# Performance work log

Measured on AMD Instinct MI355X. Metric: run time of the kernel, lower is better.

Reference implementation:

```python
import jax, jax.numpy as jnp
import numpy as np

N_NODES = 50000
N_EDGES = 600000
D_IN = 128
D_OUT = 128


def setup_inputs() -> dict:
    key = jax.random.key(0)
    ks = jax.random.split(key, 6)
    gain = float(np.sqrt(2.0))  # relu gain for xavier init
    lim = gain * np.sqrt(6.0 / (D_IN + D_IN))
    pool_w = jax.random.uniform(ks[0], (D_IN, D_IN), jnp.float32, -lim, lim)
    lim2 = gain * np.sqrt(6.0 / (D_IN + D_OUT))
    lin_w = jax.random.uniform(ks[1], (D_OUT, D_IN), jnp.float32, -lim2, lim2)
    return {
        "node_feats": jax.random.normal(ks[2], (N_NODES, D_IN), jnp.float32),
        "src": jax.random.randint(ks[3], (N_EDGES,), 0, N_NODES, jnp.int32),
        "dst": jax.random.randint(ks[4], (N_EDGES,), 0, N_NODES, jnp.int32),
        "e_weight": jax.random.uniform(ks[5], (N_EDGES,), jnp.float32),
        "pool_w": pool_w,
        "pool_b": jnp.zeros((D_IN,), jnp.float32),
        "lin_w": lin_w,
        "lin_b": jnp.zeros((D_OUT,), jnp.float32),
        "bias": jnp.zeros((D_OUT,), jnp.float32),
    }


def reference(node_feats, src, dst, e_weight, pool_w, pool_b, lin_w, lin_b, bias):
    # maxpool aggregator: h_src = relu(pool(x) + pool_bias)   [N, D_IN]
    h_src = jax.nn.relu(node_feats @ pool_w.T + pool_b)
    # u_mul_e message: gather src features, scale by edge weight  [E, D_IN]
    m = h_src[src] * e_weight[:, None]
    # fn.max reduce per destination node; empty mailboxes -> 0
    h_new = jax.ops.segment_max(m, dst, num_segments=N_NODES)
    h_new = jnp.where(jnp.isfinite(h_new), h_new, 0.0)
    # final linear (+its bias) + extra bias parameter
    return h_new @ lin_w.T + lin_b + bias
```

## Files before the change

### kernel.cpp

```cpp
#include <hip/hip_runtime.h>
#include <hip/hip_bf16.h>

#define NN 50000
#define NE 600000
#define DD 128
#define CAP 48

typedef __attribute__((ext_vector_type(8))) short short8_t;
typedef __attribute__((ext_vector_type(4))) short short4_t;
typedef __attribute__((ext_vector_type(4))) float f32x4;

__device__ __forceinline__ short f2bf(float f) {
    union { float f; unsigned u; } v; v.f = f;
    unsigned r = (v.u + 0x7FFFu + ((v.u >> 16) & 1u)) >> 16;
    return (short)r;
}
__device__ __forceinline__ float bflo(unsigned x) { return __uint_as_float(x << 16); }
__device__ __forceinline__ float bfhi(unsigned x) { return __uint_as_float(x & 0xffff0000u); }

template<bool RELU, bool B2, bool IN_BF, bool OUT_BF>
__global__ __launch_bounds__(512) void gemm128(const void* __restrict__ Av,
        const float* __restrict__ W, const float* __restrict__ b1,
        const float* __restrict__ b2, void* __restrict__ outv, int M)
{
    __shared__ short aL[128 * 128];
    __shared__ short wL[128 * 128];
    const int tid = threadIdx.x;
    const int m0 = blockIdx.x * 128;

    if (IN_BF) {
        const unsigned short* A = (const unsigned short*)Av;
        #pragma unroll
        for (int i = 0; i < 4; ++i) {
            int flat = i * 4096 + tid * 8;
            int row = flat >> 7, k = flat & 127;
            int gr = m0 + row;
            short8_t s8 = {0,0,0,0,0,0,0,0};
            if (gr < M) s8 = *(const short8_t*)(A + (size_t)gr * 128 + k);
            *(short8_t*)(aL + ((row * 128 + k) ^ ((row & 7) << 3))) = s8;
        }
    } else {
        const float* A = (const float*)Av;
        #pragma unroll
        for (int i = 0; i < 8; ++i) {
            int flat = i * 2048 + tid * 4;
            int row = flat >> 7, k = flat & 127;
            int gr = m0 + row;
            float4 v = make_float4(0.f, 0.f, 0.f, 0.f);
            if (gr < M) v = *(const float4*)(A + (size_t)gr * 128 + k);
            short4_t s4 = { f2bf(v.x), f2bf(v.y), f2bf(v.z), f2bf(v.w) };
            *(short4_t*)(aL + ((row * 128 + k) ^ ((row & 7) << 3))) = s4;
        }
    }
    #pragma unroll
    for (int i = 0; i < 8; ++i) {
        int flat = i * 2048 + tid * 4;
        int row = flat >> 7, k = flat & 127;
        float4 v = *(const float4*)(W + flat);
        short4_t s4 = { f2bf(v.x), f2bf(v.y), f2bf(v.z), f2bf(v.w) };
        *(short4_t*)(wL + ((row * 128 + k) ^ ((row & 7) << 3))) = s4;
    }
    __syncthreads();

    const int lane = tid & 63, wid = tid >> 6;
    const int l15 = lane & 15, lhi = lane >> 4;
    const int r0 = wid * 16;
    f32x4 acc[8];
    #pragma unroll
    for (int t = 0; t < 8; ++t) acc[t] = f32x4{0.f, 0.f, 0.f, 0.f};

    #pragma unroll
    for (int kk = 0; kk < 4; ++kk) {
        const int k0 = kk * 32 + lhi * 8;
        const int ar = r0 + l15;
        short8_t a = *(short8_t*)(aL + ((ar * 128 + k0) ^ ((ar & 7) << 3)));
        #pragma unroll
        for (int t = 0; t < 8; ++t) {
            const int br = t * 16 + l15;
            short8_t b = *(short8_t*)(wL + ((br * 128 + k0) ^ ((br & 7) << 3)));
            acc[t] = __builtin_amdgcn_mfma_f32_16x16x32_bf16(a, b, acc[t], 0, 0, 0);
        }
    }

    #pragma unroll
    for (int t = 0; t < 8; ++t) {
        const int c = t * 16 + l15;
        float add = b1[c];
        if (B2) add += b2[c];
        #pragma unroll
        for (int i = 0; i < 4; ++i) {
            int r = m0 + r0 + lhi * 4 + i;
            if (r < M) {
                float v = acc[t][i] + add;
                if (RELU) v = fmaxf(v, 0.f);
                if (OUT_BF) ((unsigned short*)outv)[(size_t)r * 128 + c] = (unsigned short)f2bf(v);
                else        ((float*)outv)[(size_t)r * 128 + c] = v;
            }
        }
    }
}

__global__ __launch_bounds__(256) void bucket(const int* __restrict__ src,
        const int* __restrict__ dst, const float* __restrict__ ew,
        int* __restrict__ counts, int2* __restrict__ edges)
{
    int e = blockIdx.x * 256 + threadIdx.x;
    if (e >= NE) return;
    int d = dst[e];
    int pos = atomicAdd(&counts[d], 1);
    if (pos < CAP) edges[(size_t)d * CAP + pos] = make_int2(src[e], __float_as_int(ew[e]));
}

__global__ __launch_bounds__(256) void node_max(const unsigned short* __restrict__ hb,
        const int* __restrict__ counts, const int2* __restrict__ edges,
        unsigned short* __restrict__ hnew)
{
    int node = blockIdx.x * 4 + (threadIdx.x >> 6);
    if (node >= NN) return;
    int lane = threadIdx.x & 63;
    int deg = min(counts[node], CAP);
    const int2* ep = edges + (size_t)node * CAP;
    int2 e = make_int2(0, 0);
    if (lane < deg) e = ep[lane];
    float a0 = 0.f, a1 = 0.f, b0 = 0.f, b1v = 0.f;
    for (int j = 0; j < deg; j += 16) {
        #pragma unroll
        for (int u = 0; u < 16; u += 2) {
            int i0 = j + u, i1 = j + u + 1;
            int s0 = __shfl(e.x, i0 & 63);
            int s1 = __shfl(e.x, i1 & 63);
            float w0 = __int_as_float(__shfl(e.y, i0 & 63));
            float w1 = __int_as_float(__shfl(e.y, i1 & 63));
            w0 = (i0 < deg) ? w0 : 0.f;
            w1 = (i1 < deg) ? w1 : 0.f;
            unsigned x0 = *(const unsigned*)(hb + (size_t)s0 * 128 + lane * 2);
            unsigned x1 = *(const unsigned*)(hb + (size_t)s1 * 128 + lane * 2);
            a0 = fmaxf(a0, bflo(x0) * w0); a1 = fmaxf(a1, bfhi(x0) * w0);
            b0 = fmaxf(b0, bflo(x1) * w1); b1v = fmaxf(b1v, bfhi(x1) * w1);
        }
    }
    float m0 = fmaxf(a0, b0), m1 = fmaxf(a1, b1v);
    unsigned o = ((unsigned)(unsigned short)f2bf(m1) << 16) | (unsigned short)f2bf(m0);
    *(unsigned*)(hnew + (size_t)node * 128 + lane * 2) = o;
}

extern "C" void kernel_launch(void* const* d_in, const int* in_sizes, int n_in,
                              void* d_out, int out_size, void* d_ws, size_t ws_size,
                              hipStream_t stream) {
    const float* node_feats = (const float*)d_in[0];
    const int*   src        = (const int*)d_in[1];
    const int*   dst        = (const int*)d_in[2];
    const float* ew         = (const float*)d_in[3];
    const float* pool_w     = (const float*)d_in[4];
    const float* pool_b     = (const float*)d_in[5];
    const float* lin_w      = (const float*)d_in[6];
    const float* lin_b      = (const float*)d_in[7];
    const float* bias       = (const float*)d_in[8];
    float* out = (float*)d_out;

    char* w0 = (char*)d_ws;
    unsigned short* hsrc = (unsigned short*)w0;  w0 += (size_t)NN * DD * 2;
    unsigned short* hnew = (unsigned short*)w0;  w0 += (size_t)NN * DD * 2;
    int* counts = (int*)w0;                      w0 += (size_t)NN * 4;
    int2* edges = (int2*)w0;                     w0 += (size_t)NN * CAP * 8;

    hipMemsetAsync(counts, 0, (size_t)NN * 4, stream);

    const int gemm_grid = (NN + 127) / 128;
    gemm128<true, false, false, true><<<gemm_grid, 512, 0, stream>>>(node_feats,
            pool_w, pool_b, nullptr, hsrc, NN);

    bucket<<<(NE + 255) / 256, 256, 0, stream>>>(src, dst, ew, counts, edges);

    node_max<<<(NN + 3) / 4, 256, 0, stream>>>(hsrc, counts, edges, hnew);

    gemm128<false, true, true, false><<<gemm_grid, 512, 0, stream>>>(hnew,
            lin_w, lin_b, bias, out, NN);
}
```

Measured before the change: 173.6 us.

## Pack edge records to 32 bits, vectorize gather, fold count reset into GEMM

Edge records become a single 32-bit word holding a 16-bit source index and a bf16 weight, halving bucket storage and traffic. The node max kernel splits each wave into four 16-lane groups that read 16-byte chunks, so two edges per group are handled per iteration, followed by a cross-group shuffle reduction. The count reset memset is folded into the first GEMM kernel to save a launch. Edge weights lose precision through bf16 rounding, and source indices must fit in 16 bits.

After: 167.8 us. 3.4% less time.

```diff
diff --git a/kernel.cpp b/kernel.cpp
--- a/kernel.cpp
+++ b/kernel.cpp
@@ -21,12 +21,18 @@
 template<bool RELU, bool B2, bool IN_BF, bool OUT_BF>
 __global__ __launch_bounds__(512) void gemm128(const void* __restrict__ Av,
         const float* __restrict__ W, const float* __restrict__ b1,
-        const float* __restrict__ b2, void* __restrict__ outv, int M)
+        const float* __restrict__ b2, void* __restrict__ outv, int M,
+        int* __restrict__ zbuf)
 {
     __shared__ short aL[128 * 128];
     __shared__ short wL[128 * 128];
     const int tid = threadIdx.x;
     const int m0 = blockIdx.x * 128;
+
+    if (zbuf) {
+        int gid = blockIdx.x * 512 + tid;
+        if (gid < NN) zbuf[gid] = 0;
+    }
 
     if (IN_BF) {
         const unsigned short* A = (const unsigned short*)Av;
@@ -102,46 +108,61 @@
 
 __global__ __launch_bounds__(256) void bucket(const int* __restrict__ src,
         const int* __restrict__ dst, const float* __restrict__ ew,
-        int* __restrict__ counts, int2* __restrict__ edges)
+        int* __restrict__ counts, unsigned* __restrict__ edges)
 {
     int e = blockIdx.x * 256 + threadIdx.x;
     if (e >= NE) return;
     int d = dst[e];
     int pos = atomicAdd(&counts[d], 1);
-    if (pos < CAP) edges[(size_t)d * CAP + pos] = make_int2(src[e], __float_as_int(ew[e]));
+    if (pos < CAP)
+        edges[(size_t)d * CAP + pos] =
+            ((unsigned)src[e] << 16) | (unsigned short)f2bf(ew[e]);
 }
 
 __global__ __launch_bounds__(256) void node_max(const unsigned short* __restrict__ hb,
-        const int* __restrict__ counts, const int2* __restrict__ edges,
+        const int* __restrict__ counts, const unsigned* __restrict__ edges,
         unsigned short* __restrict__ hnew)
 {
     int node = blockIdx.x * 4 + (threadIdx.x >> 6);
     if (node >= NN) return;
-    int lane = threadIdx.x & 63;
-    int deg = min(counts[node], CAP);
-    const int2* ep = edges + (size_t)node * CAP;
-    int2 e = make_int2(0, 0);
-    if (lane < deg) e = ep[lane];
-    float a0 = 0.f, a1 = 0.f, b0 = 0.f, b1v = 0.f;
-    for (int j = 0; j < deg; j += 16) {
-        #pragma unroll
-        for (int u = 0; u < 16; u += 2) {
-            int i0 = j + u, i1 = j + u + 1;
-            int s0 = __shfl(e.x, i0 & 63);
-            int s1 = __shfl(e.x, i1 & 63);
-            float w0 = __int_as_float(__shfl(e.y, i0 & 63));
-            float w1 = __int_as_float(__shfl(e.y, i1 & 63));
-            w0 = (i0 < deg) ? w0 : 0.f;
-            w1 = (i1 < deg) ? w1 : 0.f;
-            unsigned x0 = *(const unsigned*)(hb + (size_t)s0 * 128 + lane * 2);
-            unsigned x1 = *(const unsigned*)(hb + (size_t)s1 * 128 + lane * 2);
-            a0 = fmaxf(a0, bflo(x0) * w0); a1 = fmaxf(a1, bfhi(x0) * w0);
-            b0 = fmaxf(b0, bflo(x1) * w1); b1v = fmaxf(b1v, bfhi(x1) * w1);
-        }
+    const int lane = threadIdx.x & 63;
+    const int g = lane >> 4, l16 = lane & 15;
+    const int deg = min(counts[node], CAP);
+    const unsigned* ep = edges + (size_t)node * CAP;
+    unsigned p = (lane < deg) ? ep[lane] : 0u;
+
+    float m0=0.f,m1=0.f,m2=0.f,m3=0.f,m4=0.f,m5=0.f,m6=0.f,m7=0.f;
+    for (int j = 0; j < deg; j += 8) {
+        int ia = j + g, ib = j + 4 + g;
+        unsigned pa = __shfl(p, ia & 63);
+        unsigned pb = __shfl(p, ib & 63);
+        float wa = (ia < deg) ? __uint_as_float(pa << 16) : 0.f;
+        float wb = (ib < deg) ? __uint_as_float(pb << 16) : 0.f;
+        uint4 ra = *(const uint4*)(hb + (size_t)(pa >> 16) * 128 + l16 * 8);
+        uint4 rb = *(const uint4*)(hb + (size_t)(pb >> 16) * 128 + l16 * 8);
+        m0 = fmaxf(m0, bflo(ra.x) * wa); m1 = fmaxf(m1, bfhi(ra.x) * wa);
+        m2 = fmaxf(m2, bflo(ra.y) * wa); m3 = fmaxf(m3, bfhi(ra.y) * wa);
+        m4 = fmaxf(m4, bflo(ra.z) * wa); m5 = fmaxf(m5, bfhi(ra.z) * wa);
+        m6 = fmaxf(m6, bflo(ra.w) * wa); m7 = fmaxf(m7, bfhi(ra.w) * wa);
+        m0 = fmaxf(m0, bflo(rb.x) * wb); m1 = fmaxf(m1, bfhi(rb.x) * wb);
+        m2 = fmaxf(m2, bflo(rb.y) * wb); m3 = fmaxf(m3, bfhi(rb.y) * wb);
+        m4 = fmaxf(m4, bflo(rb.z) * wb); m5 = fmaxf(m5, bfhi(rb.z) * wb);
+        m6 = fmaxf(m6, bflo(rb.w) * wb); m7 = fmaxf(m7, bfhi(rb.w) * wb);
     }
-    float m0 = fmaxf(a0, b0), m1 = fmaxf(a1, b1v);
-    unsigned o = ((unsigned)(unsigned short)f2bf(m1) << 16) | (unsigned short)f2bf(m0);
-    *(unsigned*)(hnew + (size_t)node * 128 + lane * 2) = o;
+
+    #define CMB(mm) mm = fmaxf(mm, __shfl_xor(mm, 16)); \
+                    mm = fmaxf(mm, __shfl_xor(mm, 32));
+    CMB(m0) CMB(m1) CMB(m2) CMB(m3) CMB(m4) CMB(m5) CMB(m6) CMB(m7)
+    #undef CMB
+
+    if (g == 0) {
+        uint4 o;
+        o.x = ((unsigned)(unsigned short)f2bf(m1) << 16) | (unsigned short)f2bf(m0);
+        o.y = ((unsigned)(unsigned short)f2bf(m3) << 16) | (unsigned short)f2bf(m2);
+        o.z = ((unsigned)(unsigned short)f2bf(m5) << 16) | (unsigned short)f2bf(m4);
+        o.w = ((unsigned)(unsigned short)f2bf(m7) << 16) | (unsigned short)f2bf(m6);
+        *(uint4*)(hnew + (size_t)node * 128 + l16 * 8) = o;
+    }
 }
 
 extern "C" void kernel_launch(void* const* d_in, const int* in_sizes, int n_in,
@@ -162,18 +183,16 @@
     unsigned short* hsrc = (unsigned short*)w0;  w0 += (size_t)NN * DD * 2;
     unsigned short* hnew = (unsigned short*)w0;  w0 += (size_t)NN * DD * 2;
     int* counts = (int*)w0;                      w0 += (size_t)NN * 4;
-    int2* edges = (int2*)w0;                     w0 += (size_t)NN * CAP * 8;
-
-    hipMemsetAsync(counts, 0, (size_t)NN * 4, stream);
+    unsigned* edges = (unsigned*)w0;             w0 += (size_t)NN * CAP * 4;
 
     const int gemm_grid = (NN + 127) / 128;
     gemm128<true, false, false, true><<<gemm_grid, 512, 0, stream>>>(node_feats,
-            pool_w, pool_b, nullptr, hsrc, NN);
+            pool_w, pool_b, nullptr, hsrc, NN, counts);
 
     bucket<<<(NE + 255) / 256, 256, 0, stream>>>(src, dst, ew, counts, edges);
 
     node_max<<<(NN + 3) / 4, 256, 0, stream>>>(hsrc, counts, edges, hnew);
 
     gemm128<false, true, true, false><<<gemm_grid, 512, 0, stream>>>(hnew,
-            lin_w, lin_b, bias, out, NN);
+            lin_w, lin_b, bias, out, NN, nullptr);
 }
```
